# Optimization experiments

Hardware: AMD Instinct MI355X
Metric: run time of the kernel (lower is better)

Reference implementation:

```python
import jax, jax.numpy as jnp
import numpy as np

B, F = 1024, 2048
NUM_KERNELS, KERNEL_DIM = 32, 8


def setup_inputs() -> dict:
    key = jax.random.key(0)
    kx, kw = jax.random.split(key)
    x = jax.random.normal(kx, (B, F), dtype=jnp.float32)
    W = jax.random.normal(kw, (F, NUM_KERNELS * KERNEL_DIM), dtype=jnp.float32) * (1.0 / np.sqrt(F))
    return {"x": x, "W": W}


def reference(x, W):
    # Minibatch discrimination (Salimans et al. 2016), faithful to the TF layer.
    m = jnp.matmul(x, W).reshape(-1, NUM_KERNELS, KERNEL_DIM)  # [B, K, D]
    # all-pairs diffs: [B, K, D, B]
    diffs = m[:, :, :, None] - jnp.transpose(m, (1, 2, 0))[None, :, :, :]
    abs_diffs = jnp.sum(jnp.abs(diffs), axis=2)        # [B, K, B] (L1 over D)
    mb_feats = jnp.sum(jnp.exp(-abs_diffs), axis=2)    # [B, K]
    return jnp.concatenate([x, mb_feats], axis=-1)     # [B, F + K]
```

## Files before the change

kernel.cpp:

```cpp
#include <hip/hip_runtime.h>
#include <hip/hip_bf16.h>

#define B_SZ 1024
#define F_SZ 2048
#define NK   32
#define NCOL 256
#define OUTF 2080

typedef __attribute__((ext_vector_type(8))) short short8v;
typedef __attribute__((ext_vector_type(4))) float f32x4;

static __device__ __forceinline__ unsigned short f2bf(float v) {
  __hip_bfloat16 h = __float2bfloat16(v);
  return reinterpret_cast<unsigned short&>(h);
}

__global__ __launch_bounds__(512) void k1_gemm(
    const float* __restrict__ x, const float* __restrict__ W,
    float* __restrict__ m) {
  __shared__ float red[8][16][64];

  int bid = blockIdx.x;
  int mt = bid & 31, nt = bid >> 5;
  int i0 = mt * 32, n0 = nt * 32;

  int t = threadIdx.x;
  int w = t >> 6, l = t & 63;
  int hi = l >> 4;
  int r16 = l & 15;
  int hi8 = hi * 8;

  f32x4 acc[2][2];
#pragma unroll
  for (int mi = 0; mi < 2; ++mi)
#pragma unroll
    for (int ni = 0; ni < 2; ++ni) acc[mi][ni] = (f32x4)(0.f);

  for (int ks = 0; ks < 8; ++ks) {
    int kc = w * 256 + ks * 32;

    short8v af[2];
#pragma unroll
    for (int mi = 0; mi < 2; ++mi) {
      const float* ap = &x[(size_t)(i0 + mi * 16 + r16) * F_SZ + kc + hi8];
      float4 v0 = *reinterpret_cast<const float4*>(ap);
      float4 v1 = *reinterpret_cast<const float4*>(ap + 4);
      af[mi][0] = (short)f2bf(v0.x); af[mi][1] = (short)f2bf(v0.y);
      af[mi][2] = (short)f2bf(v0.z); af[mi][3] = (short)f2bf(v0.w);
      af[mi][4] = (short)f2bf(v1.x); af[mi][5] = (short)f2bf(v1.y);
      af[mi][6] = (short)f2bf(v1.z); af[mi][7] = (short)f2bf(v1.w);
    }

    short8v bfr[2];
#pragma unroll
    for (int ni = 0; ni < 2; ++ni) {
      int n = n0 + ni * 16 + r16;
      float wv[8];
#pragma unroll
      for (int u = 0; u < 8; ++u)
        wv[u] = W[(size_t)(kc + hi8 + u) * NCOL + n];
#pragma unroll
      for (int u = 0; u < 8; ++u) bfr[ni][u] = (short)f2bf(wv[u]);
    }

#pragma unroll
    for (int mi = 0; mi < 2; ++mi)
#pragma unroll
      for (int ni = 0; ni < 2; ++ni)
        acc[mi][ni] = __builtin_amdgcn_mfma_f32_16x16x32_bf16(
            af[mi], bfr[ni], acc[mi][ni], 0, 0, 0);
  }

#pragma unroll
  for (int mi = 0; mi < 2; ++mi)
#pragma unroll
    for (int ni = 0; ni < 2; ++ni)
#pragma unroll
      for (int r = 0; r < 4; ++r)
        red[w][mi * 8 + ni * 4 + r][l] = acc[mi][ni][r];
  __syncthreads();

#pragma unroll
  for (int s = 0; s < 2; ++s) {
    int slot = t + s * 512;
    int reg = slot >> 6, lane = slot & 63;
    float v = 0.f;
#pragma unroll
    for (int ww = 0; ww < 8; ++ww) v += red[ww][reg][lane];
    int mi = reg >> 3, ni = (reg >> 2) & 1, r = reg & 3;
    int row = i0 + mi * 16 + (lane >> 4) * 4 + r;
    int col = n0 + ni * 16 + (lane & 15);
    m[(size_t)row * NCOL + col] = v;
  }
}

__global__ __launch_bounds__(1024) void k2_pairwise_copy(
    const float* __restrict__ m, const float* __restrict__ x,
    float* __restrict__ out) {
  __shared__ float red[32][4][33];

  int bid = blockIdx.x;
  int t = threadIdx.x;

  if (bid >= 256) {
    const float4* x4 = reinterpret_cast<const float4*>(x);
    int idx = (bid - 256) * 1024 + t;
#pragma unroll
    for (int it = 0; it < 4; ++it, idx += 128 * 1024) {
      int i  = idx >> 9;
      int c4 = idx & 511;
      float4 v = x4[idx];
      *reinterpret_cast<float4*>(&out[(size_t)i * OUTF + c4 * 4]) = v;
    }
    return;
  }

  int k  = t & 31;
  int jc = t >> 5;
  int i0 = bid * 4;
  int j0 = jc * 32;

  const float4* mv = reinterpret_cast<const float4*>(m);
  float4 a0[4], a1[4];
#pragma unroll
  for (int r = 0; r < 4; ++r) {
    a0[r] = mv[(size_t)(i0 + r) * 64 + k * 2];
    a1[r] = mv[(size_t)(i0 + r) * 64 + k * 2 + 1];
  }

  float acc[4] = {0.f, 0.f, 0.f, 0.f};
#pragma unroll 2
  for (int jj = 0; jj < 32; ++jj) {
    int j = j0 + jj;
    float4 c0 = mv[(size_t)j * 64 + k * 2];
    float4 c1 = mv[(size_t)j * 64 + k * 2 + 1];
#pragma unroll
    for (int r = 0; r < 4; ++r) {
      float s = fabsf(a0[r].x - c0.x) + fabsf(a0[r].y - c0.y) +
                fabsf(a0[r].z - c0.z) + fabsf(a0[r].w - c0.w) +
                fabsf(a1[r].x - c1.x) + fabsf(a1[r].y - c1.y) +
                fabsf(a1[r].z - c1.z) + fabsf(a1[r].w - c1.w);
      acc[r] += __expf(-s);
    }
  }

#pragma unroll
  for (int r = 0; r < 4; ++r) red[jc][r][k] = acc[r];
  __syncthreads();

  if (t < 128) {
    int r = t >> 5, kk = t & 31;
    float s = 0.f;
#pragma unroll
    for (int c = 0; c < 32; ++c) s += red[c][r][kk];
    out[(size_t)(i0 + r) * OUTF + F_SZ + kk] = s;
  }
}

extern "C" void kernel_launch(void* const* d_in, const int* in_sizes, int n_in,
                              void* d_out, int out_size, void* d_ws, size_t ws_size,
                              hipStream_t stream) {
  const float* x = (const float*)d_in[0];
  const float* W = (const float*)d_in[1];
  float* out = (float*)d_out;
  float* m = (float*)d_ws;

  k1_gemm<<<dim3(256), 512, 0, stream>>>(x, W, m);
  k2_pairwise_copy<<<dim3(384), 1024, 0, stream>>>(m, x, out);
}
```

Measured before the change: 42.27 us.

## Pre-transpose W to bf16 in a prep kernel and move x copy there

Adds a prep kernel that converts W to bf16 and transposes it to [N, K] layout, so the GEMM can load each B fragment as one contiguous 16-byte vector instead of eight strided scalar loads with conversions. The x-to-output copy moves from the pairwise kernel into the prep kernel. The cost is a third kernel launch and an extra round trip of W through the workspace. The GEMM now depends on the prep kernel, so the copy no longer overlaps with the pairwise work.

```diff
diff --git a/kernel.cpp b/kernel.cpp
--- a/kernel.cpp
+++ b/kernel.cpp
@@ -8,6 +8,7 @@
 #define OUTF 2080
 
 typedef __attribute__((ext_vector_type(8))) short short8v;
+typedef __attribute__((ext_vector_type(8))) unsigned short ushort8v;
 typedef __attribute__((ext_vector_type(4))) float f32x4;
 
 static __device__ __forceinline__ unsigned short f2bf(float v) {
@@ -15,8 +16,53 @@
   return reinterpret_cast<unsigned short&>(h);
 }
 
+__global__ __launch_bounds__(256) void k0_prep(
+    const float* __restrict__ W, const float* __restrict__ x,
+    unsigned short* __restrict__ wt, float* __restrict__ out) {
+  int bid = blockIdx.x;
+  int t = threadIdx.x;
+
+  if (bid < 128) {
+    __shared__ unsigned short tile[64][66];
+    int kt = bid & 31, ntile = bid >> 5;
+    int k0 = kt * 64, n0 = ntile * 64;
+    int r  = t >> 2;
+    int c0 = (t & 3) * 16;
+#pragma unroll
+    for (int u = 0; u < 4; ++u) {
+      float4 v = *reinterpret_cast<const float4*>(
+          &W[(size_t)(k0 + r) * NCOL + n0 + c0 + 4 * u]);
+      tile[r][c0 + 4 * u + 0] = f2bf(v.x);
+      tile[r][c0 + 4 * u + 1] = f2bf(v.y);
+      tile[r][c0 + 4 * u + 2] = f2bf(v.z);
+      tile[r][c0 + 4 * u + 3] = f2bf(v.w);
+    }
+    __syncthreads();
+    int n  = t >> 2;
+    int kq = (t & 3) * 16;
+    ushort8v o0, o1;
+#pragma unroll
+    for (int u = 0; u < 8; ++u) o0[u] = tile[kq + u][n];
+#pragma unroll
+    for (int u = 0; u < 8; ++u) o1[u] = tile[kq + 8 + u][n];
+    unsigned short* dst = &wt[(size_t)(n0 + n) * F_SZ + k0 + kq];
+    *reinterpret_cast<ushort8v*>(dst)     = o0;
+    *reinterpret_cast<ushort8v*>(dst + 8) = o1;
+  } else {
+    const float4* x4 = reinterpret_cast<const float4*>(x);
+    int idx = (bid - 128) * 256 + t;
+#pragma unroll
+    for (int it = 0; it < 16; ++it, idx += 128 * 256) {
+      int i  = idx >> 9;
+      int c4 = idx & 511;
+      float4 v = x4[idx];
+      *reinterpret_cast<float4*>(&out[(size_t)i * OUTF + c4 * 4]) = v;
+    }
+  }
+}
+
 __global__ __launch_bounds__(512) void k1_gemm(
-    const float* __restrict__ x, const float* __restrict__ W,
+    const float* __restrict__ x, const unsigned short* __restrict__ wt,
     float* __restrict__ m) {
   __shared__ float red[8][16][64];
 
@@ -26,8 +72,7 @@
 
   int t = threadIdx.x;
   int w = t >> 6, l = t & 63;
-  int hi = l >> 4;
-  int r16 = l & 15;
+  int hi = l >> 4, r16 = l & 15;
   int hi8 = hi * 8;
 
   f32x4 acc[2][2];
@@ -53,15 +98,9 @@
 
     short8v bfr[2];
 #pragma unroll
-    for (int ni = 0; ni < 2; ++ni) {
-      int n = n0 + ni * 16 + r16;
-      float wv[8];
-#pragma unroll
-      for (int u = 0; u < 8; ++u)
-        wv[u] = W[(size_t)(kc + hi8 + u) * NCOL + n];
-#pragma unroll
-      for (int u = 0; u < 8; ++u) bfr[ni][u] = (short)f2bf(wv[u]);
-    }
+    for (int ni = 0; ni < 2; ++ni)
+      bfr[ni] = *reinterpret_cast<const short8v*>(
+          &wt[(size_t)(n0 + ni * 16 + r16) * F_SZ + kc + hi8]);
 
 #pragma unroll
     for (int mi = 0; mi < 2; ++mi)
@@ -94,27 +133,12 @@
   }
 }
 
-__global__ __launch_bounds__(1024) void k2_pairwise_copy(
-    const float* __restrict__ m, const float* __restrict__ x,
-    float* __restrict__ out) {
+__global__ __launch_bounds__(1024) void k2_pairwise(
+    const float* __restrict__ m, float* __restrict__ out) {
   __shared__ float red[32][4][33];
 
   int bid = blockIdx.x;
   int t = threadIdx.x;
-
-  if (bid >= 256) {
-    const float4* x4 = reinterpret_cast<const float4*>(x);
-    int idx = (bid - 256) * 1024 + t;
-#pragma unroll
-    for (int it = 0; it < 4; ++it, idx += 128 * 1024) {
-      int i  = idx >> 9;
-      int c4 = idx & 511;
-      float4 v = x4[idx];
-      *reinterpret_cast<float4*>(&out[(size_t)i * OUTF + c4 * 4]) = v;
-    }
-    return;
-  }
-
   int k  = t & 31;
   int jc = t >> 5;
   int i0 = bid * 4;
@@ -163,8 +187,13 @@
   const float* x = (const float*)d_in[0];
   const float* W = (const float*)d_in[1];
   float* out = (float*)d_out;
-  float* m = (float*)d_ws;
+  char* ws = (char*)d_ws;
 
-  k1_gemm<<<dim3(256), 512, 0, stream>>>(x, W, m);
-  k2_pairwise_copy<<<dim3(384), 1024, 0, stream>>>(m, x, out);
+  const size_t MB = 1u << 20;
+  unsigned short* wt = (unsigned short*)ws;
+  float* m = (float*)(ws + MB);
+
+  k0_prep<<<dim3(256), 256, 0, stream>>>(W, x, wt, out);
+  k1_gemm<<<dim3(256), 512, 0, stream>>>(x, wt, m);
+  k2_pairwise<<<dim3(256), 1024, 0, stream>>>(m, out);
 }
```

New measurement: 46.76 us. +10.6%, slower.

## Fuse GEMM and pairwise kernels into one persistent kernel with grid barriers

Applied to the files above, without the earlier changes.

Merges the two launches into a single 256-block persistent kernel that uses atomic-counter grid barriers in place of the kernel boundary. A first phase pre-transposes W into bf16 so the GEMM can use vector loads of B fragments. The x-to-out copy is placed between the barrier arrive and wait so it overlaps the wait for GEMM results. This relies on all 256 blocks being co-resident, adds a memset launch plus spin-wait overhead, and halves the pairwise parallelism per block compared with the previous 1024-thread layout.

```diff
diff --git a/kernel.cpp b/kernel.cpp
--- a/kernel.cpp
+++ b/kernel.cpp
@@ -6,8 +6,11 @@
 #define NK   32
 #define NCOL 256
 #define OUTF 2080
+#define NBLK 256
+#define NTHR 512
 
 typedef __attribute__((ext_vector_type(8))) short short8v;
+typedef __attribute__((ext_vector_type(4))) short short4v;
 typedef __attribute__((ext_vector_type(4))) float f32x4;
 
 static __device__ __forceinline__ unsigned short f2bf(float v) {
@@ -15,145 +18,171 @@
   return reinterpret_cast<unsigned short&>(h);
 }
 
-__global__ __launch_bounds__(512) void k1_gemm(
+static __device__ __forceinline__ void barrier_arrive(unsigned* c) {
+  __builtin_amdgcn_fence(__ATOMIC_RELEASE, "agent");
+  __syncthreads();
+  if (threadIdx.x == 0)
+    __hip_atomic_fetch_add(c, 1u, __ATOMIC_RELAXED, __HIP_MEMORY_SCOPE_AGENT);
+}
+static __device__ __forceinline__ void barrier_wait(unsigned* c) {
+  if (threadIdx.x == 0) {
+    for (int it = 0; it < 2000000; ++it) {
+      if (__hip_atomic_load(c, __ATOMIC_RELAXED, __HIP_MEMORY_SCOPE_AGENT) >= NBLK) break;
+      __builtin_amdgcn_s_sleep(2);
+    }
+  }
+  __syncthreads();
+  __builtin_amdgcn_fence(__ATOMIC_ACQUIRE, "agent");
+}
+
+__global__ __launch_bounds__(NTHR, 4) void mega(
     const float* __restrict__ x, const float* __restrict__ W,
-    float* __restrict__ m) {
-  __shared__ float red[8][16][64];
-
-  int bid = blockIdx.x;
-  int mt = bid & 31, nt = bid >> 5;
-  int i0 = mt * 32, n0 = nt * 32;
-
-  int t = threadIdx.x;
-  int w = t >> 6, l = t & 63;
-  int hi = l >> 4;
-  int r16 = l & 15;
-  int hi8 = hi * 8;
-
-  f32x4 acc[2][2];
-#pragma unroll
-  for (int mi = 0; mi < 2; ++mi)
-#pragma unroll
-    for (int ni = 0; ni < 2; ++ni) acc[mi][ni] = (f32x4)(0.f);
-
-  for (int ks = 0; ks < 8; ++ks) {
-    int kc = w * 256 + ks * 32;
-
-    short8v af[2];
-#pragma unroll
-    for (int mi = 0; mi < 2; ++mi) {
-      const float* ap = &x[(size_t)(i0 + mi * 16 + r16) * F_SZ + kc + hi8];
-      float4 v0 = *reinterpret_cast<const float4*>(ap);
-      float4 v1 = *reinterpret_cast<const float4*>(ap + 4);
-      af[mi][0] = (short)f2bf(v0.x); af[mi][1] = (short)f2bf(v0.y);
-      af[mi][2] = (short)f2bf(v0.z); af[mi][3] = (short)f2bf(v0.w);
-      af[mi][4] = (short)f2bf(v1.x); af[mi][5] = (short)f2bf(v1.y);
-      af[mi][6] = (short)f2bf(v1.z); af[mi][7] = (short)f2bf(v1.w);
-    }
-
-    short8v bfr[2];
-#pragma unroll
-    for (int ni = 0; ni < 2; ++ni) {
-      int n = n0 + ni * 16 + r16;
-      float wv[8];
-#pragma unroll
-      for (int u = 0; u < 8; ++u)
-        wv[u] = W[(size_t)(kc + hi8 + u) * NCOL + n];
-#pragma unroll
-      for (int u = 0; u < 8; ++u) bfr[ni][u] = (short)f2bf(wv[u]);
-    }
-
+    float* __restrict__ out, unsigned short* __restrict__ wt,
+    float* __restrict__ m, unsigned* __restrict__ ctr) {
+  __shared__ __align__(16) char smem[32768];
+  int bid = blockIdx.x, t = threadIdx.x;
+
+  {
+    typedef unsigned short tile_t[128][19];
+    tile_t& tile = *reinterpret_cast<tile_t*>(smem);
+    int kt = bid & 15, ntile = bid >> 4;
+    int k0 = kt * 128, n0 = ntile * 16;
+    int lr = t >> 4, lc = t & 15;
+#pragma unroll
+    for (int u = 0; u < 4; ++u) {
+      int row = u * 32 + lr;
+      tile[row][lc] = f2bf(W[(size_t)(k0 + row) * NCOL + n0 + lc]);
+    }
+    __syncthreads();
+    int c = t >> 5, kq = (t & 31) * 4;
+    short4v o;
+#pragma unroll
+    for (int u = 0; u < 4; ++u) o[u] = (short)tile[kq + u][c];
+    *reinterpret_cast<short4v*>(&wt[(size_t)(n0 + c) * F_SZ + k0 + kq]) = o;
+  }
+  barrier_arrive(&ctr[0]);
+  barrier_wait(&ctr[0]);
+
+  {
+    typedef float red_t[8][16][64];
+    red_t& red = *reinterpret_cast<red_t*>(smem);
+    int mt = bid & 31, nt = bid >> 5;
+    int i0 = mt * 32, n0 = nt * 32;
+    int w = t >> 6, l = t & 63;
+    int hi = l >> 4, r16 = l & 15;
+    int hi8 = hi * 8;
+
+    f32x4 acc[2][2];
 #pragma unroll
     for (int mi = 0; mi < 2; ++mi)
 #pragma unroll
+      for (int ni = 0; ni < 2; ++ni) acc[mi][ni] = (f32x4)(0.f);
+
+    for (int ks = 0; ks < 8; ++ks) {
+      int kc = w * 256 + ks * 32;
+      short8v af[2];
+#pragma unroll
+      for (int mi = 0; mi < 2; ++mi) {
+        const float* ap = &x[(size_t)(i0 + mi * 16 + r16) * F_SZ + kc + hi8];
+        float4 v0 = *reinterpret_cast<const float4*>(ap);
+        float4 v1 = *reinterpret_cast<const float4*>(ap + 4);
+        af[mi][0] = (short)f2bf(v0.x); af[mi][1] = (short)f2bf(v0.y);
+        af[mi][2] = (short)f2bf(v0.z); af[mi][3] = (short)f2bf(v0.w);
+        af[mi][4] = (short)f2bf(v1.x); af[mi][5] = (short)f2bf(v1.y);
+        af[mi][6] = (short)f2bf(v1.z); af[mi][7] = (short)f2bf(v1.w);
+      }
+      short8v bfr[2];
+#pragma unroll
       for (int ni = 0; ni < 2; ++ni)
-        acc[mi][ni] = __builtin_amdgcn_mfma_f32_16x16x32_bf16(
-            af[mi], bfr[ni], acc[mi][ni], 0, 0, 0);
-  }
-
-#pragma unroll
-  for (int mi = 0; mi < 2; ++mi)
-#pragma unroll
-    for (int ni = 0; ni < 2; ++ni)
-#pragma unroll
-      for (int r = 0; r < 4; ++r)
-        red[w][mi * 8 + ni * 4 + r][l] = acc[mi][ni][r];
-  __syncthreads();
-
-#pragma unroll
-  for (int s = 0; s < 2; ++s) {
-    int slot = t + s * 512;
-    int reg = slot >> 6, lane = slot & 63;
-    float v = 0.f;
-#pragma unroll
-    for (int ww = 0; ww < 8; ++ww) v += red[ww][reg][lane];
-    int mi = reg >> 3, ni = (reg >> 2) & 1, r = reg & 3;
-    int row = i0 + mi * 16 + (lane >> 4) * 4 + r;
-    int col = n0 + ni * 16 + (lane & 15);
-    m[(size_t)row * NCOL + col] = v;
-  }
-}
-
-__global__ __launch_bounds__(1024) void k2_pairwise_copy(
-    const float* __restrict__ m, const float* __restrict__ x,
-    float* __restrict__ out) {
-  __shared__ float red[32][4][33];
-
-  int bid = blockIdx.x;
-  int t = threadIdx.x;
-
-  if (bid >= 256) {
+        bfr[ni] = *reinterpret_cast<const short8v*>(
+            &wt[(size_t)(n0 + ni * 16 + r16) * F_SZ + kc + hi8]);
+#pragma unroll
+      for (int mi = 0; mi < 2; ++mi)
+#pragma unroll
+        for (int ni = 0; ni < 2; ++ni)
+          acc[mi][ni] = __builtin_amdgcn_mfma_f32_16x16x32_bf16(
+              af[mi], bfr[ni], acc[mi][ni], 0, 0, 0);
+    }
+
+#pragma unroll
+    for (int mi = 0; mi < 2; ++mi)
+#pragma unroll
+      for (int ni = 0; ni < 2; ++ni)
+#pragma unroll
+        for (int r = 0; r < 4; ++r)
+          red[w][mi * 8 + ni * 4 + r][l] = acc[mi][ni][r];
+    __syncthreads();
+
+#pragma unroll
+    for (int s = 0; s < 2; ++s) {
+      int slot = t + s * NTHR;
+      int reg = slot >> 6, lane = slot & 63;
+      float v = 0.f;
+#pragma unroll
+      for (int ww = 0; ww < 8; ++ww) v += red[ww][reg][lane];
+      int mi = reg >> 3, ni = (reg >> 2) & 1, r = reg & 3;
+      int row = i0 + mi * 16 + (lane >> 4) * 4 + r;
+      int col = n0 + ni * 16 + (lane & 15);
+      m[(size_t)row * NCOL + col] = v;
+    }
+  }
+  barrier_arrive(&ctr[1]);
+
+  {
     const float4* x4 = reinterpret_cast<const float4*>(x);
-    int idx = (bid - 256) * 1024 + t;
-#pragma unroll
-    for (int it = 0; it < 4; ++it, idx += 128 * 1024) {
-      int i  = idx >> 9;
-      int c4 = idx & 511;
-      float4 v = x4[idx];
-      *reinterpret_cast<float4*>(&out[(size_t)i * OUTF + c4 * 4]) = v;
-    }
-    return;
-  }
-
-  int k  = t & 31;
-  int jc = t >> 5;
-  int i0 = bid * 4;
-  int j0 = jc * 32;
-
-  const float4* mv = reinterpret_cast<const float4*>(m);
-  float4 a0[4], a1[4];
-#pragma unroll
-  for (int r = 0; r < 4; ++r) {
-    a0[r] = mv[(size_t)(i0 + r) * 64 + k * 2];
-    a1[r] = mv[(size_t)(i0 + r) * 64 + k * 2 + 1];
-  }
-
-  float acc[4] = {0.f, 0.f, 0.f, 0.f};
+    int idx = bid * 2048 + t;
+#pragma unroll
+    for (int it = 0; it < 4; ++it, idx += NTHR) {
+      int i = idx >> 9, c4 = idx & 511;
+      *reinterpret_cast<float4*>(&out[(size_t)i * OUTF + c4 * 4]) = x4[idx];
+    }
+  }
+  barrier_wait(&ctr[1]);
+
+  {
+    typedef float red2_t[16][4][33];
+    red2_t& red2 = *reinterpret_cast<red2_t*>(smem);
+    int k  = t & 31;
+    int jc = t >> 5;
+    int i0 = bid * 4;
+    int j0 = jc * 64;
+
+    const float4* mv = reinterpret_cast<const float4*>(m);
+    float4 a0[4], a1[4];
+#pragma unroll
+    for (int r = 0; r < 4; ++r) {
+      a0[r] = mv[(size_t)(i0 + r) * 64 + k * 2];
+      a1[r] = mv[(size_t)(i0 + r) * 64 + k * 2 + 1];
+    }
+
+    float acc[4] = {0.f, 0.f, 0.f, 0.f};
 #pragma unroll 2
-  for (int jj = 0; jj < 32; ++jj) {
-    int j = j0 + jj;
-    float4 c0 = mv[(size_t)j * 64 + k * 2];
-    float4 c1 = mv[(size_t)j * 64 + k * 2 + 1];
-#pragma unroll
-    for (int r = 0; r < 4; ++r) {
-      float s = fabsf(a0[r].x - c0.x) + fabsf(a0[r].y - c0.y) +
-                fabsf(a0[r].z - c0.z) + fabsf(a0[r].w - c0.w) +
-                fabsf(a1[r].x - c1.x) + fabsf(a1[r].y - c1.y) +
-                fabsf(a1[r].z - c1.z) + fabsf(a1[r].w - c1.w);
-      acc[r] += __expf(-s);
-    }
-  }
-
-#pragma unroll
-  for (int r = 0; r < 4; ++r) red[jc][r][k] = acc[r];
-  __syncthreads();
-
-  if (t < 128) {
-    int r = t >> 5, kk = t & 31;
-    float s = 0.f;
-#pragma unroll
-    for (int c = 0; c < 32; ++c) s += red[c][r][kk];
-    out[(size_t)(i0 + r) * OUTF + F_SZ + kk] = s;
+    for (int jj = 0; jj < 64; ++jj) {
+      int j = j0 + jj;
+      float4 c0 = mv[(size_t)j * 64 + k * 2];
+      float4 c1 = mv[(size_t)j * 64 + k * 2 + 1];
+#pragma unroll
+      for (int r = 0; r < 4; ++r) {
+        float s = fabsf(a0[r].x - c0.x) + fabsf(a0[r].y - c0.y) +
+                  fabsf(a0[r].z - c0.z) + fabsf(a0[r].w - c0.w) +
+                  fabsf(a1[r].x - c1.x) + fabsf(a1[r].y - c1.y) +
+                  fabsf(a1[r].z - c1.z) + fabsf(a1[r].w - c1.w);
+        acc[r] += __expf(-s);
+      }
+    }
+
+    __syncthreads();
+#pragma unroll
+    for (int r = 0; r < 4; ++r) red2[jc][r][k] = acc[r];
+    __syncthreads();
+
+    if (t < 128) {
+      int r = t >> 5, kk = t & 31;
+      float s = 0.f;
+#pragma unroll
+      for (int c = 0; c < 16; ++c) s += red2[c][r][kk];
+      out[(size_t)(i0 + r) * OUTF + F_SZ + kk] = s;
+    }
   }
 }
 
@@ -163,8 +192,13 @@
   const float* x = (const float*)d_in[0];
   const float* W = (const float*)d_in[1];
   float* out = (float*)d_out;
-  float* m = (float*)d_ws;
-
-  k1_gemm<<<dim3(256), 512, 0, stream>>>(x, W, m);
-  k2_pairwise_copy<<<dim3(384), 1024, 0, stream>>>(m, x, out);
-}
+  char* ws = (char*)d_ws;
+
+  const size_t MB = 1u << 20;
+  unsigned short* wt = (unsigned short*)ws;
+  float* m = (float*)(ws + MB);
+  unsigned* ctr = (unsigned*)(ws + 2 * MB);
+
+  hipMemsetAsync(ctr, 0, 16, stream);
+  mega<<<dim3(NBLK), NTHR, 0, stream>>>(x, W, out, wt, m, ctr);
+}
```

Result: slower. 156.4 us (+270.1%).

## Exploit pairwise symmetry with block-pair tiles and move x copy into GEMM

Applied to the files above, without the earlier changes.

The pairwise L1/exp stage now iterates only over upper-triangular 32x32 row-block pairs and uses each exp value for both i and j, roughly halving the exp and abs work. Partial sums go to a workspace buffer and a new third kernel reduces them into the output. The copy of x into the output moves from the pairwise kernel into the GEMM launch. The cost is an extra kernel launch, shared-memory accumulation of the transposed partials, and extra global traffic for the partial buffer.

```diff
diff --git a/kernel.cpp b/kernel.cpp
--- a/kernel.cpp
+++ b/kernel.cpp
@@ -15,19 +15,30 @@
   return reinterpret_cast<unsigned short&>(h);
 }
 
-__global__ __launch_bounds__(512) void k1_gemm(
+__global__ __launch_bounds__(512) void k1_gemm_copy(
     const float* __restrict__ x, const float* __restrict__ W,
-    float* __restrict__ m) {
+    float* __restrict__ m, float* __restrict__ out) {
   __shared__ float red[8][16][64];
 
   int bid = blockIdx.x;
+  int t = threadIdx.x;
+
+  if (bid >= 256) {
+    const float4* x4 = reinterpret_cast<const float4*>(x);
+    int idx = (bid - 256) * 512 + t;
+#pragma unroll
+    for (int it = 0; it < 8; ++it, idx += 128 * 512) {
+      int i  = idx >> 9;
+      int c4 = idx & 511;
+      *reinterpret_cast<float4*>(&out[(size_t)i * OUTF + c4 * 4]) = x4[idx];
+    }
+    return;
+  }
+
   int mt = bid & 31, nt = bid >> 5;
   int i0 = mt * 32, n0 = nt * 32;
-
-  int t = threadIdx.x;
   int w = t >> 6, l = t & 63;
-  int hi = l >> 4;
-  int r16 = l & 15;
+  int hi = l >> 4, r16 = l & 15;
   int hi8 = hi * 8;
 
   f32x4 acc[2][2];
@@ -94,67 +105,75 @@
   }
 }
 
-__global__ __launch_bounds__(1024) void k2_pairwise_copy(
-    const float* __restrict__ m, const float* __restrict__ x,
-    float* __restrict__ out) {
-  __shared__ float red[32][4][33];
+__global__ __launch_bounds__(512) void k2_sym_pairwise(
+    const float* __restrict__ m, float* __restrict__ P) {
+  __shared__ float accJ[32][33];
 
-  int bid = blockIdx.x;
+  int b = blockIdx.x;
+  int a = 0, rem = b;
+  while (rem >= 32 - a) { rem -= 32 - a; ++a; }
+  int c = a + rem;
+  bool offd = (a != c);
+
   int t = threadIdx.x;
+  int ig = t & 15, k = t >> 4;
 
-  if (bid >= 256) {
-    const float4* x4 = reinterpret_cast<const float4*>(x);
-    int idx = (bid - 256) * 1024 + t;
-#pragma unroll
-    for (int it = 0; it < 4; ++it, idx += 128 * 1024) {
-      int i  = idx >> 9;
-      int c4 = idx & 511;
-      float4 v = x4[idx];
-      *reinterpret_cast<float4*>(&out[(size_t)i * OUTF + c4 * 4]) = v;
-    }
-    return;
+  for (int e = t; e < 32 * 33; e += 512) ((float*)accJ)[e] = 0.f;
+  __syncthreads();
+
+  const float4* mv = reinterpret_cast<const float4*>(m);
+  int ia = a * 32 + ig * 2;
+  float4 A00 = mv[(size_t)ia * 64 + k * 2];
+  float4 A01 = mv[(size_t)ia * 64 + k * 2 + 1];
+  float4 A10 = mv[(size_t)(ia + 1) * 64 + k * 2];
+  float4 A11 = mv[(size_t)(ia + 1) * 64 + k * 2 + 1];
+
+  float accI0 = 0.f, accI1 = 0.f;
+#pragma unroll 2
+  for (int jj = 0; jj < 32; ++jj) {
+    int jr = (jj + 2 * ig) & 31;
+    int j = c * 32 + jr;
+    float4 C0 = mv[(size_t)j * 64 + k * 2];
+    float4 C1 = mv[(size_t)j * 64 + k * 2 + 1];
+    float s0 = fabsf(A00.x - C0.x) + fabsf(A00.y - C0.y) +
+               fabsf(A00.z - C0.z) + fabsf(A00.w - C0.w) +
+               fabsf(A01.x - C1.x) + fabsf(A01.y - C1.y) +
+               fabsf(A01.z - C1.z) + fabsf(A01.w - C1.w);
+    float s1 = fabsf(A10.x - C0.x) + fabsf(A10.y - C0.y) +
+               fabsf(A10.z - C0.z) + fabsf(A10.w - C0.w) +
+               fabsf(A11.x - C1.x) + fabsf(A11.y - C1.y) +
+               fabsf(A11.z - C1.z) + fabsf(A11.w - C1.w);
+    float e0 = __expf(-s0);
+    float e1 = __expf(-s1);
+    accI0 += e0;
+    accI1 += e1;
+    if (offd) accJ[jr][k] += e0 + e1;
   }
 
-  int k  = t & 31;
-  int jc = t >> 5;
-  int i0 = bid * 4;
-  int j0 = jc * 32;
+  P[(((size_t)a * 32 + c) * 32 + ig * 2)     * 32 + k] = accI0;
+  P[(((size_t)a * 32 + c) * 32 + ig * 2 + 1) * 32 + k] = accI1;
 
-  const float4* mv = reinterpret_cast<const float4*>(m);
-  float4 a0[4], a1[4];
+  if (offd) {
+    __syncthreads();
 #pragma unroll
-  for (int r = 0; r < 4; ++r) {
-    a0[r] = mv[(size_t)(i0 + r) * 64 + k * 2];
-    a1[r] = mv[(size_t)(i0 + r) * 64 + k * 2 + 1];
-  }
-
-  float acc[4] = {0.f, 0.f, 0.f, 0.f};
-#pragma unroll 2
-  for (int jj = 0; jj < 32; ++jj) {
-    int j = j0 + jj;
-    float4 c0 = mv[(size_t)j * 64 + k * 2];
-    float4 c1 = mv[(size_t)j * 64 + k * 2 + 1];
-#pragma unroll
-    for (int r = 0; r < 4; ++r) {
-      float s = fabsf(a0[r].x - c0.x) + fabsf(a0[r].y - c0.y) +
-                fabsf(a0[r].z - c0.z) + fabsf(a0[r].w - c0.w) +
-                fabsf(a1[r].x - c1.x) + fabsf(a1[r].y - c1.y) +
-                fabsf(a1[r].z - c1.z) + fabsf(a1[r].w - c1.w);
-      acc[r] += __expf(-s);
+    for (int s = 0; s < 2; ++s) {
+      int e = t + s * 512;
+      int jr = e >> 5, kk = e & 31;
+      P[(((size_t)c * 32 + a) * 32 + jr) * 32 + kk] = accJ[jr][kk];
     }
   }
+}
 
+__global__ __launch_bounds__(256) void k3_finalize(
+    const float* __restrict__ P, float* __restrict__ out) {
+  int g = blockIdx.x * 256 + threadIdx.x;
+  int i = g >> 5, k = g & 31;
+  int aa = i >> 5, ir = i & 31;
+  float s = 0.f;
 #pragma unroll
-  for (int r = 0; r < 4; ++r) red[jc][r][k] = acc[r];
-  __syncthreads();
-
-  if (t < 128) {
-    int r = t >> 5, kk = t & 31;
-    float s = 0.f;
-#pragma unroll
-    for (int c = 0; c < 32; ++c) s += red[c][r][kk];
-    out[(size_t)(i0 + r) * OUTF + F_SZ + kk] = s;
-  }
+  for (int sl = 0; sl < 32; ++sl)
+    s += P[(((size_t)aa * 32 + sl) * 32 + ir) * 32 + k];
+  out[(size_t)i * OUTF + F_SZ + k] = s;
 }
 
 extern "C" void kernel_launch(void* const* d_in, const int* in_sizes, int n_in,
@@ -163,8 +182,13 @@
   const float* x = (const float*)d_in[0];
   const float* W = (const float*)d_in[1];
   float* out = (float*)d_out;
-  float* m = (float*)d_ws;
+  char* ws = (char*)d_ws;
 
-  k1_gemm<<<dim3(256), 512, 0, stream>>>(x, W, m);
-  k2_pairwise_copy<<<dim3(384), 1024, 0, stream>>>(m, x, out);
+  const size_t MB = 1u << 20;
+  float* m = (float*)ws;
+  float* P = (float*)(ws + MB);
+
+  k1_gemm_copy<<<dim3(384), 512, 0, stream>>>(x, W, m, out);
+  k2_sym_pairwise<<<dim3(528), 512, 0, stream>>>(m, P);
+  k3_finalize<<<dim3(128), 256, 0, stream>>>(P, out);
 }
```

Result: slower. 69.09 us (+63.5%).
